# Kernel optimization log

Hardware: AMD Instinct MI355X
Metric: run time of the kernel (lower is better)

## Reference

```python
import jax, jax.numpy as jnp
import numpy as np

D_MODEL = 1024
NUM_HEADS = 16
HEAD_DIM = D_MODEL // NUM_HEADS


def setup_inputs() -> dict:
    key = jax.random.key(0)
    ks = jax.random.split(key, 11)
    B, S, D = 2, 2048, D_MODEL
    s = 1.0 / np.sqrt(D)
    return {
        "query": jax.random.normal(ks[0], (B, S, D), jnp.float32),
        "key": jax.random.normal(ks[1], (B, S, D), jnp.float32),
        "value": jax.random.normal(ks[2], (B, S, D), jnp.float32),
        "W_q": jax.random.normal(ks[3], (D, D), jnp.float32) * s,
        "b_q": jnp.zeros((D,), jnp.float32),
        "W_k": jax.random.normal(ks[4], (D, D), jnp.float32) * s,
        "b_k": jnp.zeros((D,), jnp.float32),
        "W_v": jax.random.normal(ks[5], (D, D), jnp.float32) * s,
        "b_v": jnp.zeros((D,), jnp.float32),
        "W_o": jax.random.normal(ks[6], (D, D), jnp.float32) * s,
        "b_o": jnp.zeros((D,), jnp.float32),
    }


def reference(query, key, value, W_q, b_q, W_k, b_k, W_v, b_v, W_o, b_o):
    B, S, D = query.shape
    H, Dh = NUM_HEADS, HEAD_DIM
    # linear projections then split heads: [B, S, D] -> [B, H, S, Dh]
    def split_heads(x):
        return x.reshape(B, -1, H, Dh).transpose(0, 2, 1, 3)
    Q = split_heads(query @ W_q.T + b_q)
    K = split_heads(key @ W_k.T + b_k)
    V = split_heads(value @ W_v.T + b_v)
    # NOTE: original scales by d_model**-0.5, not head_dim**-0.5
    scale = jnp.asarray(D, Q.dtype) ** -0.5
    scores = jnp.einsum("bhqd,bhkd->bhqk", Q, K) * scale
    attn = jax.nn.softmax(scores, axis=-1)  # includes max-subtraction stabilization
    out = jnp.einsum("bhqk,bhkd->bhqd", attn, V)
    out = out.transpose(0, 2, 1, 3).reshape(B, -1, D)
    return out @ W_o.T + b_o
```

## Files before the change

kernel.cpp:

```cpp
#include <hip/hip_runtime.h>
#include <stdint.h>


typedef unsigned short u16;
typedef short s16x8 __attribute__((ext_vector_type(8)));
typedef short s16x4 __attribute__((ext_vector_type(4)));
typedef float f32x4 __attribute__((ext_vector_type(4)));
typedef u16 u16x4 __attribute__((ext_vector_type(4)));

#define S_LEN 2048
#define DMODEL 1024
#define LOG2E 1.44269504088896340736f

__device__ __forceinline__ u16 f2bf(float f) {
  union { float f; uint32_t u; } v; v.f = f;
  return (u16)((v.u + 0x8000u) >> 16);
}

__device__ __forceinline__ s16x8 ld8f(const float* s) {
  f32x4 a = *(const f32x4*)s;
  f32x4 b = *(const f32x4*)(s + 4);
  s16x8 r;
  r[0] = (short)f2bf(a[0]); r[1] = (short)f2bf(a[1]);
  r[2] = (short)f2bf(a[2]); r[3] = (short)f2bf(a[3]);
  r[4] = (short)f2bf(b[0]); r[5] = (short)f2bf(b[1]);
  r[6] = (short)f2bf(b[2]); r[7] = (short)f2bf(b[3]);
  return r;
}

__device__ __forceinline__ void gl2lds16(const u16* g, u16* l) {
  __builtin_amdgcn_global_load_lds(
      (const __attribute__((address_space(1))) uint32_t*)g,
      (__attribute__((address_space(3))) uint32_t*)l, 16, 0, 0);
}

struct Cvt7 { const float* s[7]; u16* d[7]; int n[7]; };

__global__ __launch_bounds__(256) void cvt7(Cvt7 p) {
  const int z = blockIdx.y;
  const int idx = blockIdx.x * 256 + threadIdx.x;
  if (idx * 8 < p.n[z])
    *(s16x8*)(p.d[z] + (size_t)idx * 8) = ld8f(p.s[z] + (size_t)idx * 8);
}

struct GemmBatch {
  const u16* A[3]; const u16* W[3]; const float* Bv[3]; void* C[3];
};

template <bool OUT_F32>
__global__ __launch_bounds__(256) void gemm_bt(GemmBatch p, int M, int N, int K) {
  __shared__ u16 As[128 * 64];
  __shared__ u16 Ws[128 * 64];
  const int z = blockIdx.z;
  const u16* __restrict__ A      = p.A[z];
  const u16* __restrict__ W      = p.W[z];
  const float* __restrict__ bias = p.Bv[z];

  const int tid = threadIdx.x;
  const int wave = tid >> 6, lane = tid & 63;
  const int quad = lane >> 4, l16 = lane & 15;
  const int bm = blockIdx.y * 128, bn = blockIdx.x * 128;
  const int wr = (wave >> 1) * 64, wc = (wave & 1) * 64;
  const int sr8 = lane >> 3;
  const int slc = (lane & 7) ^ sr8;
  const int srow = wave * 8 + sr8;

  f32x4 acc[4][4];
#pragma unroll
  for (int i = 0; i < 4; i++)
#pragma unroll
    for (int j = 0; j < 4; j++) acc[i][j] = {0.f, 0.f, 0.f, 0.f};

  const u16* Ab = A + (size_t)bm * K;
  const u16* Wb = W + (size_t)bn * K;

  for (int kt = 0; kt < K; kt += 64) {
    __syncthreads();
#pragma unroll
    for (int i = 0; i < 4; i++)
      gl2lds16(Ab + (size_t)(i * 32 + srow) * K + kt + slc * 8,
               &As[(i * 32 + wave * 8) * 64]);
#pragma unroll
    for (int i = 0; i < 4; i++)
      gl2lds16(Wb + (size_t)(i * 32 + srow) * K + kt + slc * 8,
               &Ws[(i * 32 + wave * 8) * 64]);
    __syncthreads();

#pragma unroll
    for (int ks = 0; ks < 2; ks++) {
      const int ch = ks * 4 + quad;
      s16x8 a[4], b[4];
#pragma unroll
      for (int t = 0; t < 4; t++)
        a[t] = *(const s16x8*)&As[(wr + t * 16 + l16) * 64 + ((ch ^ (l16 & 7)) << 3)];
#pragma unroll
      for (int t = 0; t < 4; t++)
        b[t] = *(const s16x8*)&Ws[(wc + t * 16 + l16) * 64 + ((ch ^ (l16 & 7)) << 3)];
#pragma unroll
      for (int i = 0; i < 4; i++)
#pragma unroll
        for (int j = 0; j < 4; j++)
          acc[i][j] = __builtin_amdgcn_mfma_f32_16x16x32_bf16(a[i], b[j], acc[i][j], 0, 0, 0);
    }
  }

#pragma unroll
  for (int j = 0; j < 4; j++) {
    const int col = bn + wc + j * 16 + l16;
    const float bv = bias[col];
#pragma unroll
    for (int i = 0; i < 4; i++) {
      const int row0 = bm + wr + i * 16 + quad * 4;
#pragma unroll
      for (int r = 0; r < 4; r++) {
        const float val = acc[i][j][r] + bv;
        if (OUT_F32)
          ((float*)p.C[z])[(size_t)(row0 + r) * N + col] = val;
        else
          ((u16*)p.C[z])[(size_t)(row0 + r) * N + col] = f2bf(val);
      }
    }
  }
}

__global__ __launch_bounds__(256) void transpose_v(const u16* __restrict__ Vp,
                                                   u16* __restrict__ Vt) {
  __shared__ u16 t[64 * 72];
  const int tid = threadIdx.x;
  const int bh = blockIdx.y, b = bh >> 4, h = bh & 15;
  const int s0 = blockIdx.x * 64;
  const int r = tid >> 4, c4 = (tid & 15) * 4;
#pragma unroll
  for (int i = 0; i < 4; i++) {
    const int s = i * 16 + r;
    u16x4 v = *(const u16x4*)&Vp[(size_t)(b * S_LEN + s0 + s) * DMODEL + h * 64 + c4];
    *(u16x4*)&t[s * 72 + c4] = v;
  }
  __syncthreads();
#pragma unroll
  for (int i = 0; i < 4; i++) {
    const int d = i * 16 + r;
    u16x4 v;
    v.x = t[(c4 + 0) * 72 + d];
    v.y = t[(c4 + 1) * 72 + d];
    v.z = t[(c4 + 2) * 72 + d];
    v.w = t[(c4 + 3) * 72 + d];
    *(u16x4*)&Vt[(size_t)(bh * 64 + d) * S_LEN + s0 + c4] = v;
  }
}

__global__ __launch_bounds__(256, 2) void attn_kernel(const u16* __restrict__ Qp,
                                                      const u16* __restrict__ Kp,
                                                      const u16* __restrict__ Vt,
                                                      u16* __restrict__ AO) {
  __shared__ u16 Qs[128 * 64];
  __shared__ u16 Ks[128 * 64];
  __shared__ u16 Vs[64 * 128];

  const int tid = threadIdx.x;
  const int wave = tid >> 6, lane = tid & 63;
  const int quad = lane >> 4, l16 = lane & 15;
  const int bh = blockIdx.y, b = bh >> 4, h = bh & 15;
  const int s0 = blockIdx.x * 128;
  const float c = 0.03125f * LOG2E;

  const int qr = lane >> 3, qc = lane & 7;
  const int vd = lane >> 4, vc = lane & 15;

#pragma unroll
  for (int i = 0; i < 4; i++) {
    const int rr = i * 32 + wave * 8 + qr;
    s16x8 qv = *(const s16x8*)(Qp + (size_t)(b * S_LEN + s0 + rr) * DMODEL + h * 64 + qc * 8);
    *(s16x8*)&Qs[rr * 64 + ((qc ^ qr) << 3)] = qv;
  }
  __syncthreads();

  s16x8 aq[2][2];
#pragma unroll
  for (int ks = 0; ks < 2; ks++)
#pragma unroll
    for (int rt = 0; rt < 2; rt++) {
      const int row = wave * 32 + rt * 16 + l16;
      const int ch = ks * 4 + quad;
      aq[ks][rt] = *(const s16x8*)&Qs[row * 64 + ((ch ^ (l16 & 7)) << 3)];
    }

  s16x8 kv[4], vv[4];
#pragma unroll
  for (int i = 0; i < 4; i++) {
    const int rr = i * 32 + wave * 8 + qr;
    kv[i] = *(const s16x8*)(Kp + (size_t)(b * S_LEN + rr) * DMODEL + h * 64 + qc * 8);
  }
#pragma unroll
  for (int i = 0; i < 4; i++) {
    const int dd = i * 16 + wave * 4 + vd;
    vv[i] = *(const s16x8*)(Vt + (size_t)(bh * 64 + dd) * S_LEN + vc * 8);
  }

  f32x4 o[2][4];
  float l_r[2] = {0.f, 0.f};
#pragma unroll
  for (int rt = 0; rt < 2; rt++)
#pragma unroll
    for (int dt = 0; dt < 4; dt++) o[rt][dt] = {0.f, 0.f, 0.f, 0.f};

  const f32x4 zf = {0.f, 0.f, 0.f, 0.f};

  for (int kt = 0; kt < S_LEN; kt += 128) {
    __syncthreads();
#pragma unroll
    for (int i = 0; i < 4; i++) {
      const int rr = i * 32 + wave * 8 + qr;
      *(s16x8*)&Ks[rr * 64 + ((qc ^ qr) << 3)] = kv[i];
    }
#pragma unroll
    for (int i = 0; i < 4; i++) {
      const int dd = i * 16 + wave * 4 + vd;
      *(s16x8*)&Vs[dd * 128 + ((vc ^ (dd & 15)) << 3)] = vv[i];
    }
    __syncthreads();

    if (kt + 128 < S_LEN) {
      const int k2 = kt + 128;
#pragma unroll
      for (int i = 0; i < 4; i++) {
        const int rr = i * 32 + wave * 8 + qr;
        kv[i] = *(const s16x8*)(Kp + (size_t)(b * S_LEN + k2 + rr) * DMODEL + h * 64 + qc * 8);
      }
#pragma unroll
      for (int i = 0; i < 4; i++) {
        const int dd = i * 16 + wave * 4 + vd;
        vv[i] = *(const s16x8*)(Vt + (size_t)(bh * 64 + dd) * S_LEN + k2 + vc * 8);
      }
    }

#pragma unroll
    for (int kvt = 0; kvt < 8; kvt++) {
      const int krow = kvt * 16 + l16;
      s16x8 ak0 = *(const s16x8*)&Ks[krow * 64 + (((0 + quad) ^ (l16 & 7)) << 3)];
      s16x8 ak1 = *(const s16x8*)&Ks[krow * 64 + (((4 + quad) ^ (l16 & 7)) << 3)];
      f32x4 sA, sB;
      sA = __builtin_amdgcn_mfma_f32_16x16x32_bf16(ak0, aq[0][0], zf, 0, 0, 0);
      sA = __builtin_amdgcn_mfma_f32_16x16x32_bf16(ak1, aq[1][0], sA, 0, 0, 0);
      sB = __builtin_amdgcn_mfma_f32_16x16x32_bf16(ak0, aq[0][1], zf, 0, 0, 0);
      sB = __builtin_amdgcn_mfma_f32_16x16x32_bf16(ak1, aq[1][1], sB, 0, 0, 0);

      s16x4 pf0, pf1;
      float rs0 = 0.f, rs1 = 0.f;
#pragma unroll
      for (int r = 0; r < 4; r++) {
        const float p0 = exp2f(sA[r] * c);
        const float p1 = exp2f(sB[r] * c);
        rs0 += p0; rs1 += p1;
        pf0[r] = (short)f2bf(p0);
        pf1[r] = (short)f2bf(p1);
      }
      l_r[0] += rs0; l_r[1] += rs1;

      const int ch = kvt * 2 + (quad >> 1);
#pragma unroll
      for (int dt = 0; dt < 4; dt++) {
        const int row = dt * 16 + l16;
        s16x4 bv = *(const s16x4*)&Vs[row * 128 + ((ch ^ l16) << 3) + (quad & 1) * 4];
        o[0][dt] = __builtin_amdgcn_mfma_f32_16x16x16bf16_1k(pf0, bv, o[0][dt], 0, 0, 0);
        o[1][dt] = __builtin_amdgcn_mfma_f32_16x16x16bf16_1k(pf1, bv, o[1][dt], 0, 0, 0);
      }
    }
  }

#pragma unroll
  for (int rt = 0; rt < 2; rt++) {
    l_r[rt] += __shfl_xor(l_r[rt], 16);
    l_r[rt] += __shfl_xor(l_r[rt], 32);
  }
#pragma unroll
  for (int rt = 0; rt < 2; rt++) {
#pragma unroll
    for (int r = 0; r < 4; r++) {
      const float linv = 1.f / __shfl(l_r[rt], quad * 4 + r);
      const int row = s0 + wave * 32 + rt * 16 + quad * 4 + r;
#pragma unroll
      for (int dt = 0; dt < 4; dt++)
        AO[(size_t)(b * S_LEN + row) * DMODEL + h * 64 + dt * 16 + l16] =
            f2bf(o[rt][dt][r] * linv);
    }
  }
}

extern "C" void kernel_launch(void* const* d_in, const int* in_sizes, int n_in,
                              void* d_out, int out_size, void* d_ws, size_t ws_size,
                              hipStream_t stream) {
  const float* query = (const float*)d_in[0];
  const float* key_  = (const float*)d_in[1];
  const float* value = (const float*)d_in[2];
  const float* W_q = (const float*)d_in[3];
  const float* b_q = (const float*)d_in[4];
  const float* W_k = (const float*)d_in[5];
  const float* b_k = (const float*)d_in[6];
  const float* W_v = (const float*)d_in[7];
  const float* b_v = (const float*)d_in[8];
  const float* W_o = (const float*)d_in[9];
  const float* b_o = (const float*)d_in[10];
  float* out = (float*)d_out;

  const int M = 2 * S_LEN;
  const int N = DMODEL, K = DMODEL;
  const size_t WSZ = (size_t)DMODEL * DMODEL;
  const size_t SZ  = (size_t)M * DMODEL;

  u16* Wqb = (u16*)d_ws;
  u16* Wkb = Wqb + WSZ;
  u16* Wvb = Wkb + WSZ;
  u16* Wob = Wvb + WSZ;
  u16* Qa  = Wob + WSZ;
  u16* Ka  = Qa + SZ;
  u16* Va  = Ka + SZ;
  u16* Qp  = Va + SZ;
  u16* Kp  = Qp + SZ;
  u16* Vp  = Kp + SZ;
  u16* Vt  = Qa;
  u16* AO  = Qp;

  Cvt7 cw;
  cw.s[0] = W_q;   cw.d[0] = Wqb; cw.n[0] = (int)WSZ;
  cw.s[1] = W_k;   cw.d[1] = Wkb; cw.n[1] = (int)WSZ;
  cw.s[2] = W_v;   cw.d[2] = Wvb; cw.n[2] = (int)WSZ;
  cw.s[3] = W_o;   cw.d[3] = Wob; cw.n[3] = (int)WSZ;
  cw.s[4] = query; cw.d[4] = Qa;  cw.n[4] = (int)SZ;
  cw.s[5] = key_;  cw.d[5] = Ka;  cw.n[5] = (int)SZ;
  cw.s[6] = value; cw.d[6] = Va;  cw.n[6] = (int)SZ;
  cvt7<<<dim3((int)(SZ / 2048), 7), 256, 0, stream>>>(cw);

  GemmBatch p1;
  p1.A[0] = Qa; p1.W[0] = Wqb; p1.Bv[0] = b_q; p1.C[0] = Qp;
  p1.A[1] = Ka; p1.W[1] = Wkb; p1.Bv[1] = b_k; p1.C[1] = Kp;
  p1.A[2] = Va; p1.W[2] = Wvb; p1.Bv[2] = b_v; p1.C[2] = Vp;
  gemm_bt<false><<<dim3(N / 128, M / 128, 3), 256, 0, stream>>>(p1, M, N, K);

  transpose_v<<<dim3(S_LEN / 64, 32), 256, 0, stream>>>(Vp, Vt);

  attn_kernel<<<dim3(S_LEN / 128, 32), 256, 0, stream>>>(Qp, Kp, Vt, AO);

  GemmBatch p2;
  p2.A[0] = AO; p2.W[0] = Wob; p2.Bv[0] = b_o; p2.C[0] = out;
  p2.A[1] = AO; p2.W[1] = Wob; p2.Bv[1] = b_o; p2.C[1] = out;
  p2.A[2] = AO; p2.W[2] = Wob; p2.Bv[2] = b_o; p2.C[2] = out;
  gemm_bt<true><<<dim3(N / 128, M / 128, 1), 256, 0, stream>>>(p2, M, N, K);
}
```

Baseline: 261.5 us.

## Split attention block across 8 waves with 16 query rows each

The attention kernel now runs with 512 threads per block instead of 256. Each wave handles 16 query rows instead of 32, and the K/V tile staging is spread across twice as many threads. The aim is more waves in flight to hide the LDS and global-load latency of the exp and MFMA loop. In exchange, K fragments read from LDS are reused across fewer MFMAs and there are more waves per barrier, which raises LDS read traffic per unit of compute.

```diff
diff --git a/kernel.cpp b/kernel.cpp
--- a/kernel.cpp
+++ b/kernel.cpp
@@ -149,7 +149,7 @@
   }
 }
 
-__global__ __launch_bounds__(256, 2) void attn_kernel(const u16* __restrict__ Qp,
+__global__ __launch_bounds__(512, 2) void attn_kernel(const u16* __restrict__ Qp,
                                                       const u16* __restrict__ Kp,
                                                       const u16* __restrict__ Vt,
                                                       u16* __restrict__ AO) {
@@ -164,74 +164,59 @@
   const int s0 = blockIdx.x * 128;
   const float c = 0.03125f * LOG2E;
 
-  const int qr = lane >> 3, qc = lane & 7;
-  const int vd = lane >> 4, vc = lane & 15;
-
-#pragma unroll
-  for (int i = 0; i < 4; i++) {
-    const int rr = i * 32 + wave * 8 + qr;
-    s16x8 qv = *(const s16x8*)(Qp + (size_t)(b * S_LEN + s0 + rr) * DMODEL + h * 64 + qc * 8);
-    *(s16x8*)&Qs[rr * 64 + ((qc ^ qr) << 3)] = qv;
+  const int sr = tid >> 3, sc8 = tid & 7;
+  const int sxor = (sc8 ^ (sr & 7)) << 3;
+  const int vr = tid >> 4, vc = tid & 15;
+  const int vxor = (vc ^ (vr & 15)) << 3;
+
+#pragma unroll
+  for (int i = 0; i < 2; i++) {
+    const int rr = i * 64 + sr;
+    s16x8 qv = *(const s16x8*)(Qp + (size_t)(b * S_LEN + s0 + rr) * DMODEL + h * 64 + sc8 * 8);
+    *(s16x8*)&Qs[rr * 64 + sxor] = qv;
   }
   __syncthreads();
 
-  s16x8 aq[2][2];
-#pragma unroll
-  for (int ks = 0; ks < 2; ks++)
-#pragma unroll
-    for (int rt = 0; rt < 2; rt++) {
-      const int row = wave * 32 + rt * 16 + l16;
-      const int ch = ks * 4 + quad;
-      aq[ks][rt] = *(const s16x8*)&Qs[row * 64 + ((ch ^ (l16 & 7)) << 3)];
-    }
-
-  s16x8 kv[4], vv[4];
-#pragma unroll
-  for (int i = 0; i < 4; i++) {
-    const int rr = i * 32 + wave * 8 + qr;
-    kv[i] = *(const s16x8*)(Kp + (size_t)(b * S_LEN + rr) * DMODEL + h * 64 + qc * 8);
-  }
-#pragma unroll
-  for (int i = 0; i < 4; i++) {
-    const int dd = i * 16 + wave * 4 + vd;
-    vv[i] = *(const s16x8*)(Vt + (size_t)(bh * 64 + dd) * S_LEN + vc * 8);
-  }
-
-  f32x4 o[2][4];
-  float l_r[2] = {0.f, 0.f};
-#pragma unroll
-  for (int rt = 0; rt < 2; rt++)
-#pragma unroll
-    for (int dt = 0; dt < 4; dt++) o[rt][dt] = {0.f, 0.f, 0.f, 0.f};
+  s16x8 aq[2];
+#pragma unroll
+  for (int ks = 0; ks < 2; ks++) {
+    const int ch = ks * 4 + quad;
+    aq[ks] = *(const s16x8*)&Qs[(wave * 16 + l16) * 64 + ((ch ^ (l16 & 7)) << 3)];
+  }
+
+  s16x8 kv[2], vv[2];
+#pragma unroll
+  for (int i = 0; i < 2; i++)
+    kv[i] = *(const s16x8*)(Kp + (size_t)(b * S_LEN + i * 64 + sr) * DMODEL + h * 64 + sc8 * 8);
+#pragma unroll
+  for (int i = 0; i < 2; i++)
+    vv[i] = *(const s16x8*)(Vt + (size_t)(bh * 64 + i * 32 + vr) * S_LEN + vc * 8);
+
+  f32x4 o[4];
+  float l_r = 0.f;
+#pragma unroll
+  for (int dt = 0; dt < 4; dt++) o[dt] = {0.f, 0.f, 0.f, 0.f};
 
   const f32x4 zf = {0.f, 0.f, 0.f, 0.f};
 
   for (int kt = 0; kt < S_LEN; kt += 128) {
     __syncthreads();
 #pragma unroll
-    for (int i = 0; i < 4; i++) {
-      const int rr = i * 32 + wave * 8 + qr;
-      *(s16x8*)&Ks[rr * 64 + ((qc ^ qr) << 3)] = kv[i];
-    }
-#pragma unroll
-    for (int i = 0; i < 4; i++) {
-      const int dd = i * 16 + wave * 4 + vd;
-      *(s16x8*)&Vs[dd * 128 + ((vc ^ (dd & 15)) << 3)] = vv[i];
-    }
+    for (int i = 0; i < 2; i++)
+      *(s16x8*)&Ks[(i * 64 + sr) * 64 + sxor] = kv[i];
+#pragma unroll
+    for (int i = 0; i < 2; i++)
+      *(s16x8*)&Vs[(i * 32 + vr) * 128 + vxor] = vv[i];
     __syncthreads();
 
     if (kt + 128 < S_LEN) {
       const int k2 = kt + 128;
 #pragma unroll
-      for (int i = 0; i < 4; i++) {
-        const int rr = i * 32 + wave * 8 + qr;
-        kv[i] = *(const s16x8*)(Kp + (size_t)(b * S_LEN + k2 + rr) * DMODEL + h * 64 + qc * 8);
-      }
-#pragma unroll
-      for (int i = 0; i < 4; i++) {
-        const int dd = i * 16 + wave * 4 + vd;
-        vv[i] = *(const s16x8*)(Vt + (size_t)(bh * 64 + dd) * S_LEN + k2 + vc * 8);
-      }
+      for (int i = 0; i < 2; i++)
+        kv[i] = *(const s16x8*)(Kp + (size_t)(b * S_LEN + k2 + i * 64 + sr) * DMODEL + h * 64 + sc8 * 8);
+#pragma unroll
+      for (int i = 0; i < 2; i++)
+        vv[i] = *(const s16x8*)(Vt + (size_t)(bh * 64 + i * 32 + vr) * S_LEN + k2 + vc * 8);
     }
 
 #pragma unroll
@@ -239,51 +224,40 @@
       const int krow = kvt * 16 + l16;
       s16x8 ak0 = *(const s16x8*)&Ks[krow * 64 + (((0 + quad) ^ (l16 & 7)) << 3)];
       s16x8 ak1 = *(const s16x8*)&Ks[krow * 64 + (((4 + quad) ^ (l16 & 7)) << 3)];
-      f32x4 sA, sB;
-      sA = __builtin_amdgcn_mfma_f32_16x16x32_bf16(ak0, aq[0][0], zf, 0, 0, 0);
-      sA = __builtin_amdgcn_mfma_f32_16x16x32_bf16(ak1, aq[1][0], sA, 0, 0, 0);
-      sB = __builtin_amdgcn_mfma_f32_16x16x32_bf16(ak0, aq[0][1], zf, 0, 0, 0);
-      sB = __builtin_amdgcn_mfma_f32_16x16x32_bf16(ak1, aq[1][1], sB, 0, 0, 0);
-
-      s16x4 pf0, pf1;
-      float rs0 = 0.f, rs1 = 0.f;
+      f32x4 sA;
+      sA = __builtin_amdgcn_mfma_f32_16x16x32_bf16(ak0, aq[0], zf, 0, 0, 0);
+      sA = __builtin_amdgcn_mfma_f32_16x16x32_bf16(ak1, aq[1], sA, 0, 0, 0);
+
+      s16x4 pf;
+      float rs = 0.f;
 #pragma unroll
       for (int r = 0; r < 4; r++) {
         const float p0 = exp2f(sA[r] * c);
-        const float p1 = exp2f(sB[r] * c);
-        rs0 += p0; rs1 += p1;
-        pf0[r] = (short)f2bf(p0);
-        pf1[r] = (short)f2bf(p1);
+        rs += p0;
+        pf[r] = (short)f2bf(p0);
       }
-      l_r[0] += rs0; l_r[1] += rs1;
+      l_r += rs;
 
       const int ch = kvt * 2 + (quad >> 1);
 #pragma unroll
       for (int dt = 0; dt < 4; dt++) {
         const int row = dt * 16 + l16;
         s16x4 bv = *(const s16x4*)&Vs[row * 128 + ((ch ^ l16) << 3) + (quad & 1) * 4];
-        o[0][dt] = __builtin_amdgcn_mfma_f32_16x16x16bf16_1k(pf0, bv, o[0][dt], 0, 0, 0);
-        o[1][dt] = __builtin_amdgcn_mfma_f32_16x16x16bf16_1k(pf1, bv, o[1][dt], 0, 0, 0);
+        o[dt] = __builtin_amdgcn_mfma_f32_16x16x16bf16_1k(pf, bv, o[dt], 0, 0, 0);
       }
     }
   }
 
-#pragma unroll
-  for (int rt = 0; rt < 2; rt++) {
-    l_r[rt] += __shfl_xor(l_r[rt], 16);
-    l_r[rt] += __shfl_xor(l_r[rt], 32);
-  }
-#pragma unroll
-  for (int rt = 0; rt < 2; rt++) {
-#pragma unroll
-    for (int r = 0; r < 4; r++) {
-      const float linv = 1.f / __shfl(l_r[rt], quad * 4 + r);
-      const int row = s0 + wave * 32 + rt * 16 + quad * 4 + r;
-#pragma unroll
-      for (int dt = 0; dt < 4; dt++)
-        AO[(size_t)(b * S_LEN + row) * DMODEL + h * 64 + dt * 16 + l16] =
-            f2bf(o[rt][dt][r] * linv);
-    }
+  l_r += __shfl_xor(l_r, 16);
+  l_r += __shfl_xor(l_r, 32);
+#pragma unroll
+  for (int r = 0; r < 4; r++) {
+    const float linv = 1.f / __shfl(l_r, quad * 4 + r);
+    const int row = s0 + wave * 16 + quad * 4 + r;
+#pragma unroll
+    for (int dt = 0; dt < 4; dt++)
+      AO[(size_t)(b * S_LEN + row) * DMODEL + h * 64 + dt * 16 + l16] =
+          f2bf(o[dt][r] * linv);
   }
 }
 
@@ -339,7 +313,7 @@
 
   transpose_v<<<dim3(S_LEN / 64, 32), 256, 0, stream>>>(Vp, Vt);
 
-  attn_kernel<<<dim3(S_LEN / 128, 32), 256, 0, stream>>>(Qp, Kp, Vt, AO);
+  attn_kernel<<<dim3(S_LEN / 128, 32), 512, 0, stream>>>(Qp, Kp, Vt, AO);
 
   GemmBatch p2;
   p2.A[0] = AO; p2.W[0] = Wob; p2.Bv[0] = b_o; p2.C[0] = out;
```

Result: faster. 255.1 us (-2.4%).
